# Kernel tuning notes

Hardware: AMD Instinct MI355X
Metric: run time of the kernel (lower is better)

## Reference

```python
import jax, jax.numpy as jnp
import numpy as np


def setup_inputs() -> dict:
    key = jax.random.key(0)
    B, M, S, H, D = 1, 32768, 512, 8, 64
    ks = jax.random.split(key, 5)
    f = lambda k, shape: jax.random.normal(k, shape, dtype=jnp.float32)
    return {
        "mem_keys": f(ks[0], (B, M, H, D)),
        "mem_vals": f(ks[1], (B, M, H, D)),
        "keys": f(ks[2], (B, S, H, D)),
        "values": f(ks[3], (B, S, H, D)),
        "queries": f(ks[4], (B, S, H, D)),
        "start_of_sequence": jnp.zeros((B,), dtype=jnp.bool_),
        "write_index": 0,
    }


def reference(mem_keys, mem_vals, keys, values, queries, start_of_sequence, write_index):
    """DenseKVMemory: start_segment (clear), read (joint attention), end_segment (scatter write).

    Returns (y, new_mem_keys, new_mem_vals, new_write_index).
    """
    B, S, H, D = keys.shape
    M = mem_keys.shape[1]
    dtype = mem_keys.dtype

    # --- start_segment: clear memory at document boundaries ---
    keep = jnp.logical_not(start_of_sequence).astype(dtype).reshape(B, 1, 1, 1)
    mem_keys_c = mem_keys * keep
    mem_vals_c = mem_vals * keep

    # --- read: joint attention over [memory (no mask), segment (causal mask)] ---
    scale = float(D) ** -0.5  # default 1/sqrt(head_size) when attention_scale_factor is None
    q = queries * jnp.asarray(scale, dtype)
    mem_logits = jnp.einsum('bqhd,bkhd->bhqk', q, mem_keys_c)  # [B,H,S,M]
    seg_logits = jnp.einsum('bqhd,bkhd->bhqk', q, keys)        # [B,H,S,S]

    # kq_pos = key_pos - (query_pos + queries_offset); queries_offset = 0 at segment start.
    # causal_mask True (kq_pos < 0): key strictly before query -> allowed.
    kq_pos = jnp.arange(S)[None, :] - jnp.arange(S)[:, None]
    causal_mask = kq_pos < 0  # [S,S]
    neg_inf = jnp.asarray(jnp.finfo(dtype).min, dtype)
    seg_logits = jnp.where(causal_mask[None, None, :, :], seg_logits, neg_inf)

    all_logits = jnp.concatenate([mem_logits, seg_logits], axis=-1)  # [B,H,S,M+S]
    weights = jax.nn.softmax(all_logits, axis=-1)
    all_vals = jnp.concatenate([mem_vals_c, values], axis=1)         # [B,M+S,H,D]
    y = jnp.einsum('bhqk,bkhd->bqhd', weights, all_vals)             # [B,S,H,D]

    # --- end_segment: scatter-write segment KV into the ring buffer ---
    wi = jnp.asarray(write_index, jnp.int32)
    new_mem_keys = jax.lax.dynamic_update_slice_in_dim(mem_keys_c, keys, wi, axis=1)
    new_mem_vals = jax.lax.dynamic_update_slice_in_dim(mem_vals_c, values, wi, axis=1)
    new_write_index = (wi + S) % M
    return (y, new_mem_keys, new_mem_vals, new_write_index)
```

## Files before the change

### kernel.cpp

```cpp
#include <hip/hip_runtime.h>
#include <hip/hip_bf16.h>

typedef __bf16 bf16x8 __attribute__((ext_vector_type(8)));
typedef __bf16 bf16x4 __attribute__((ext_vector_type(4)));
typedef __bf16 bf16x2 __attribute__((ext_vector_type(2)));
typedef float f32x4 __attribute__((ext_vector_type(4)));

#define M_MEM 32768
#define S_SEG 512
#define H_ 8
#define D_ 64
#define NKEY 33280
#define NTILES 520
#define LOG2E 1.44269504088896340736f
#define CMAX (14.0f * LOG2E)

#define Y_OFF 0
#define NK_OFF 262144
#define WI_OFF (262144 + 2 * 16777216)

__global__ __launch_bounds__(256, 4) void fused_attn(
    const float* __restrict__ memk, const float* __restrict__ memv,
    const float* __restrict__ keys, const float* __restrict__ vals,
    const float* __restrict__ qry, const unsigned char* __restrict__ sos,
    const int* __restrict__ wip, float* __restrict__ out,
    float* __restrict__ opart, float* __restrict__ lst, int NC) {
  const int bid = blockIdx.x;
  const int tid = threadIdx.x;
  const int c = bid >> 6;
  const int qt = (bid >> 3) & 7;
  const int h = bid & 7;
  const int w = tid >> 6;
  const int lane = tid & 63;
  const int L = lane & 15;
  const int quad = lane >> 4;
  const float keep = sos[0] ? 0.0f : 1.0f;

  int wi_raw = wip[0];
  int wi = wi_raw < 0 ? 0 : (wi_raw > M_MEM - S_SEG ? M_MEM - S_SEG : wi_raw);
  if (bid == 0 && tid == 0) {
    int nwi = (int)(((long long)wi_raw + S_SEG) % M_MEM);
    if (nwi < 0) nwi += M_MEM;
    out[WI_OFF] = (float)nwi;
  }

  __shared__ __align__(16) __bf16 Ks[64 * 72];
  __shared__ __align__(16) __bf16 Vt[64 * 72];
  __shared__ __align__(16) __bf16 Pt[4][16 * 64];

  const int qrow_base = qt * 64 + w * 16;
  const int q_abs = qrow_base + L;

  bf16x8 qf[2];
  {
    const float* qp = qry + ((size_t)q_abs * H_ + h) * D_;
    const float qs = 0.125f * LOG2E;
#pragma unroll
    for (int kb = 0; kb < 2; ++kb) {
      const int d = kb * 32 + quad * 8;
      float4 x0 = *(const float4*)(qp + d);
      float4 x1 = *(const float4*)(qp + d + 4);
      bf16x8 f;
      f[0] = (__bf16)(x0.x * qs); f[1] = (__bf16)(x0.y * qs);
      f[2] = (__bf16)(x0.z * qs); f[3] = (__bf16)(x0.w * qs);
      f[4] = (__bf16)(x1.x * qs); f[5] = (__bf16)(x1.y * qs);
      f[6] = (__bf16)(x1.z * qs); f[7] = (__bf16)(x1.w * qs);
      qf[kb] = f;
    }
  }

  f32x4 acc[4];
#pragma unroll
  for (int g = 0; g < 4; ++g) acc[g] = (f32x4){0.f, 0.f, 0.f, 0.f};
  float l_acc = 0.f;

  const int tile_start = (NTILES * c) / NC;
  const int tile_end = (NTILES * (c + 1)) / NC;
  const int nt = tile_end - tile_start;

  const int kk = tid >> 2;
  const int d0 = (tid & 3) * 16;
  const int vp2 = tid & 31;
  const int dvb = (tid >> 5) * 8;

  float4 kreg[4], vreg[4];
  float mult;
  auto issue = [&](int t) {
    const int tb = (tile_start + t) * 64;
    const float *kb_, *vb_;
    if (tb < M_MEM) {
      kb_ = memk + (size_t)tb * 512 + h * 64;
      vb_ = memv + (size_t)tb * 512 + h * 64;
      mult = keep;
    } else {
      kb_ = keys + (size_t)(tb - M_MEM) * 512 + h * 64;
      vb_ = vals + (size_t)(tb - M_MEM) * 512 + h * 64;
      mult = 1.0f;
    }
    const float* ks = kb_ + (size_t)kk * 512 + d0;
#pragma unroll
    for (int i = 0; i < 4; ++i) kreg[i] = *(const float4*)(ks + i * 4);
    const float* vs = vb_ + (size_t)(2 * vp2) * 512 + dvb;
    vreg[0] = *(const float4*)(vs);
    vreg[1] = *(const float4*)(vs + 4);
    vreg[2] = *(const float4*)(vs + 512);
    vreg[3] = *(const float4*)(vs + 516);
  };

  issue(0);
  for (int t = 0; t < nt; ++t) {
    const int tb = (tile_start + t) * 64;
    const float mu = mult;
    {
      bf16x8 lo, hi;
      lo[0] = (__bf16)(kreg[0].x * mu); lo[1] = (__bf16)(kreg[0].y * mu);
      lo[2] = (__bf16)(kreg[0].z * mu); lo[3] = (__bf16)(kreg[0].w * mu);
      lo[4] = (__bf16)(kreg[1].x * mu); lo[5] = (__bf16)(kreg[1].y * mu);
      lo[6] = (__bf16)(kreg[1].z * mu); lo[7] = (__bf16)(kreg[1].w * mu);
      hi[0] = (__bf16)(kreg[2].x * mu); hi[1] = (__bf16)(kreg[2].y * mu);
      hi[2] = (__bf16)(kreg[2].z * mu); hi[3] = (__bf16)(kreg[2].w * mu);
      hi[4] = (__bf16)(kreg[3].x * mu); hi[5] = (__bf16)(kreg[3].y * mu);
      hi[6] = (__bf16)(kreg[3].z * mu); hi[7] = (__bf16)(kreg[3].w * mu);
      *(bf16x8*)&Ks[kk * 72 + d0] = lo;
      *(bf16x8*)&Ks[kk * 72 + d0 + 8] = hi;
      const int col = (2 * vp2 + dvb) & 63;
      float a0[8] = {vreg[0].x, vreg[0].y, vreg[0].z, vreg[0].w,
                     vreg[1].x, vreg[1].y, vreg[1].z, vreg[1].w};
      float a1[8] = {vreg[2].x, vreg[2].y, vreg[2].z, vreg[2].w,
                     vreg[3].x, vreg[3].y, vreg[3].z, vreg[3].w};
#pragma unroll
      for (int i = 0; i < 8; ++i) {
        bf16x2 pr;
        pr[0] = (__bf16)(a0[i] * mu);
        pr[1] = (__bf16)(a1[i] * mu);
        *(bf16x2*)&Vt[(dvb + i) * 72 + col] = pr;
      }
      if ((((unsigned)(tb >> 6)) & 7u) == (unsigned)qt) {
        int krow = (tb < M_MEM) ? tb + kk : wi + (tb - M_MEM) + kk;
        bool kskip = (tb < M_MEM) && (krow >= wi && krow < wi + S_SEG);
        if (!kskip) {
          float* dK = out + NK_OFF + (size_t)krow * 512 + h * 64 + d0;
#pragma unroll
          for (int i = 0; i < 4; ++i) {
            float4 vv = kreg[i];
            vv.x *= mu; vv.y *= mu; vv.z *= mu; vv.w *= mu;
            *(float4*)(dK + i * 4) = vv;
          }
        }
        int r0 = (tb < M_MEM) ? tb + 2 * vp2 : wi + (tb - M_MEM) + 2 * vp2;
#pragma unroll
        for (int pk2 = 0; pk2 < 2; ++pk2) {
          int vrow = r0 + pk2;
          bool vskip = (tb < M_MEM) && (vrow >= wi && vrow < wi + S_SEG);
          if (!vskip) {
            float* dV = out + NK_OFF + 16777216 + (size_t)vrow * 512 + h * 64 + dvb;
            float4 u0 = vreg[pk2 * 2], u1 = vreg[pk2 * 2 + 1];
            u0.x *= mu; u0.y *= mu; u0.z *= mu; u0.w *= mu;
            *(float4*)(dV) = u0;
            *(float4*)(dV + 4) = u1;
          }
        }
      }
    }
    __syncthreads();
    if (t + 1 < nt) issue(t + 1);

    f32x4 sg[4];
#pragma unroll
    for (int g = 0; g < 4; ++g) {
      bf16x8 klo = *(bf16x8*)&Ks[(g * 16 + L) * 72 + quad * 8];
      bf16x8 khi = *(bf16x8*)&Ks[(g * 16 + L) * 72 + 32 + quad * 8];
      f32x4 z = (f32x4){0.f, 0.f, 0.f, 0.f};
      z = __builtin_amdgcn_mfma_f32_16x16x32_bf16(klo, qf[0], z, 0, 0, 0);
      sg[g] = __builtin_amdgcn_mfma_f32_16x16x32_bf16(khi, qf[1], z, 0, 0, 0);
    }

    const int prot = 8 * (L & 7);
#pragma unroll
    for (int g = 0; g < 4; ++g) {
      bf16x4 pk;
#pragma unroll
      for (int r = 0; r < 4; ++r) {
        const int kidx = tb + g * 16 + quad * 4 + r;
        float p = __builtin_amdgcn_exp2f(sg[g][r] - CMAX);
        const bool msk = (kidx >= M_MEM) && (kidx - M_MEM >= q_abs);
        p = msk ? 0.f : p;
        l_acc += p;
        pk[r] = (__bf16)p;
      }
      *(bf16x4*)&Pt[w][L * 64 + ((g * 16 + quad * 4 + prot) & 63)] = pk;
    }

    bf16x8 pb0 = *(bf16x8*)&Pt[w][L * 64 + ((quad * 8 + prot) & 63)];
    bf16x8 pb1 = *(bf16x8*)&Pt[w][L * 64 + ((32 + quad * 8 + prot) & 63)];
#pragma unroll
    for (int g = 0; g < 4; ++g) {
      const int vrot = g * 16 + 8 * (L >> 3);
      bf16x8 v0 = *(bf16x8*)&Vt[(g * 16 + L) * 72 + ((quad * 8 + vrot) & 63)];
      bf16x8 v1 = *(bf16x8*)&Vt[(g * 16 + L) * 72 + ((32 + quad * 8 + vrot) & 63)];
      acc[g] = __builtin_amdgcn_mfma_f32_16x16x32_bf16(v0, pb0, acc[g], 0, 0, 0);
      acc[g] = __builtin_amdgcn_mfma_f32_16x16x32_bf16(v1, pb1, acc[g], 0, 0, 0);
    }
    __syncthreads();
  }

  l_acc += __shfl_xor(l_acc, 16);
  l_acc += __shfl_xor(l_acc, 32);
  const size_t row = (size_t)h * S_SEG + q_abs;
#pragma unroll
  for (int g = 0; g < 4; ++g)
    *(f32x4*)&opart[(row * NC + c) * 64 + g * 16 + quad * 4] = acc[g];
  if (quad == 0) lst[row * NC + c] = l_acc;
}

__global__ __launch_bounds__(256) void combine(
    const float* __restrict__ opart, const float* __restrict__ lst,
    float* __restrict__ y, int NC) {
  const int idx = blockIdx.x * 256 + threadIdx.x;
  const int d = idx & 63;
  const int h = (idx >> 6) & 7;
  const int q = idx >> 9;
  const size_t row = (size_t)h * S_SEG + q;
  float num = 0.f, den = 0.f;
  for (int c = 0; c < NC; ++c) {
    num += opart[(row * NC + c) * 64 + d];
    den += lst[row * NC + c];
  }
  y[idx] = num / den;
}

extern "C" void kernel_launch(void* const* d_in, const int* in_sizes, int n_in,
                              void* d_out, int out_size, void* d_ws, size_t ws_size,
                              hipStream_t stream) {
  const float* memk = (const float*)d_in[0];
  const float* memv = (const float*)d_in[1];
  const float* keys = (const float*)d_in[2];
  const float* vals = (const float*)d_in[3];
  const float* qry  = (const float*)d_in[4];
  const unsigned char* sos = (const unsigned char*)d_in[5];
  const int* wip = (const int*)d_in[6];
  float* out = (float*)d_out;

  static const int cand[] = {20, 16, 10, 8, 5, 4, 2, 1};
  int NC = 1;
  for (int i = 0; i < 8; ++i) {
    size_t need = (size_t)cand[i] *
        ((size_t)H_ * S_SEG * D_ * 4 + (size_t)H_ * S_SEG * 4);
    if (need <= ws_size) { NC = cand[i]; break; }
  }

  float* opart = (float*)d_ws;
  float* lstp = opart + (size_t)H_ * S_SEG * NC * D_;

  fused_attn<<<NC * 64, 256, 0, stream>>>(
      memk, memv, keys, vals, qry, sos, wip, out, opart, lstp, NC);

  combine<<<1024, 256, 0, stream>>>(opart, lstp, out + Y_OFF, NC);
}
```

Baseline: 353.0 us.

## Process two query tiles per block to halve K/V tile loads

Each block now computes attention for 128 query rows (two 64-row groups) against every K/V tile it stages, so the key/value reads and bf16 conversions into shared memory are shared by twice as many queries. The grid uses half as many query blocks and allows more KV-split chunks (up to 40) to keep the GPU filled, with launch bounds relaxed to 3 to leave room for the doubled accumulators. A branch writes zeros to shared memory when memory is cleared instead of multiplying by the keep factor. Costs include higher register pressure, more partial results for the combine kernel, and an extra LDS wait between the two probability passes.

Result: faster. 326.4 us (-7.5%).

```diff
diff --git a/kernel.cpp b/kernel.cpp
--- a/kernel.cpp
+++ b/kernel.cpp
@@ -19,7 +19,7 @@
 #define NK_OFF 262144
 #define WI_OFF (262144 + 2 * 16777216)
 
-__global__ __launch_bounds__(256, 4) void fused_attn(
+__global__ __launch_bounds__(256, 3) void fused_attn(
     const float* __restrict__ memk, const float* __restrict__ memv,
     const float* __restrict__ keys, const float* __restrict__ vals,
     const float* __restrict__ qry, const unsigned char* __restrict__ sos,
@@ -27,8 +27,8 @@
     float* __restrict__ opart, float* __restrict__ lst, int NC) {
   const int bid = blockIdx.x;
   const int tid = threadIdx.x;
-  const int c = bid >> 6;
-  const int qt = (bid >> 3) & 7;
+  const int c = bid >> 5;
+  const int qp = (bid >> 3) & 3;
   const int h = bid & 7;
   const int w = tid >> 6;
   const int lane = tid & 63;
@@ -48,31 +48,41 @@
   __shared__ __align__(16) __bf16 Vt[64 * 72];
   __shared__ __align__(16) __bf16 Pt[4][16 * 64];
 
-  const int qrow_base = qt * 64 + w * 16;
-  const int q_abs = qrow_base + L;
-
-  bf16x8 qf[2];
+  const int qA = qp * 128 + w * 16 + L;
+  const int qB = qA + 64;
+
+  bf16x8 qfA[2], qfB[2];
   {
-    const float* qp = qry + ((size_t)q_abs * H_ + h) * D_;
     const float qs = 0.125f * LOG2E;
+    const float* qpA = qry + ((size_t)qA * H_ + h) * D_;
+    const float* qpB = qry + ((size_t)qB * H_ + h) * D_;
 #pragma unroll
     for (int kb = 0; kb < 2; ++kb) {
       const int d = kb * 32 + quad * 8;
-      float4 x0 = *(const float4*)(qp + d);
-      float4 x1 = *(const float4*)(qp + d + 4);
-      bf16x8 f;
-      f[0] = (__bf16)(x0.x * qs); f[1] = (__bf16)(x0.y * qs);
-      f[2] = (__bf16)(x0.z * qs); f[3] = (__bf16)(x0.w * qs);
-      f[4] = (__bf16)(x1.x * qs); f[5] = (__bf16)(x1.y * qs);
-      f[6] = (__bf16)(x1.z * qs); f[7] = (__bf16)(x1.w * qs);
-      qf[kb] = f;
-    }
-  }
-
-  f32x4 acc[4];
-#pragma unroll
-  for (int g = 0; g < 4; ++g) acc[g] = (f32x4){0.f, 0.f, 0.f, 0.f};
-  float l_acc = 0.f;
+      float4 a0 = *(const float4*)(qpA + d);
+      float4 a1 = *(const float4*)(qpA + d + 4);
+      float4 b0 = *(const float4*)(qpB + d);
+      float4 b1 = *(const float4*)(qpB + d + 4);
+      bf16x8 fa, fb;
+      fa[0] = (__bf16)(a0.x * qs); fa[1] = (__bf16)(a0.y * qs);
+      fa[2] = (__bf16)(a0.z * qs); fa[3] = (__bf16)(a0.w * qs);
+      fa[4] = (__bf16)(a1.x * qs); fa[5] = (__bf16)(a1.y * qs);
+      fa[6] = (__bf16)(a1.z * qs); fa[7] = (__bf16)(a1.w * qs);
+      fb[0] = (__bf16)(b0.x * qs); fb[1] = (__bf16)(b0.y * qs);
+      fb[2] = (__bf16)(b0.z * qs); fb[3] = (__bf16)(b0.w * qs);
+      fb[4] = (__bf16)(b1.x * qs); fb[5] = (__bf16)(b1.y * qs);
+      fb[6] = (__bf16)(b1.z * qs); fb[7] = (__bf16)(b1.w * qs);
+      qfA[kb] = fa; qfB[kb] = fb;
+    }
+  }
+
+  f32x4 accA[4], accB[4];
+#pragma unroll
+  for (int g = 0; g < 4; ++g) {
+    accA[g] = (f32x4){0.f, 0.f, 0.f, 0.f};
+    accB[g] = (f32x4){0.f, 0.f, 0.f, 0.f};
+  }
+  float lA = 0.f, lB = 0.f;
 
   const int tile_start = (NTILES * c) / NC;
   const int tile_end = (NTILES * (c + 1)) / NC;
@@ -111,16 +121,16 @@
   for (int t = 0; t < nt; ++t) {
     const int tb = (tile_start + t) * 64;
     const float mu = mult;
-    {
+    if (mu != 0.0f) {
       bf16x8 lo, hi;
-      lo[0] = (__bf16)(kreg[0].x * mu); lo[1] = (__bf16)(kreg[0].y * mu);
-      lo[2] = (__bf16)(kreg[0].z * mu); lo[3] = (__bf16)(kreg[0].w * mu);
-      lo[4] = (__bf16)(kreg[1].x * mu); lo[5] = (__bf16)(kreg[1].y * mu);
-      lo[6] = (__bf16)(kreg[1].z * mu); lo[7] = (__bf16)(kreg[1].w * mu);
-      hi[0] = (__bf16)(kreg[2].x * mu); hi[1] = (__bf16)(kreg[2].y * mu);
-      hi[2] = (__bf16)(kreg[2].z * mu); hi[3] = (__bf16)(kreg[2].w * mu);
-      hi[4] = (__bf16)(kreg[3].x * mu); hi[5] = (__bf16)(kreg[3].y * mu);
-      hi[6] = (__bf16)(kreg[3].z * mu); hi[7] = (__bf16)(kreg[3].w * mu);
+      lo[0] = (__bf16)kreg[0].x; lo[1] = (__bf16)kreg[0].y;
+      lo[2] = (__bf16)kreg[0].z; lo[3] = (__bf16)kreg[0].w;
+      lo[4] = (__bf16)kreg[1].x; lo[5] = (__bf16)kreg[1].y;
+      lo[6] = (__bf16)kreg[1].z; lo[7] = (__bf16)kreg[1].w;
+      hi[0] = (__bf16)kreg[2].x; hi[1] = (__bf16)kreg[2].y;
+      hi[2] = (__bf16)kreg[2].z; hi[3] = (__bf16)kreg[2].w;
+      hi[4] = (__bf16)kreg[3].x; hi[5] = (__bf16)kreg[3].y;
+      hi[6] = (__bf16)kreg[3].z; hi[7] = (__bf16)kreg[3].w;
       *(bf16x8*)&Ks[kk * 72 + d0] = lo;
       *(bf16x8*)&Ks[kk * 72 + d0 + 8] = hi;
       const int col = (2 * vp2 + dvb) & 63;
@@ -131,86 +141,132 @@
 #pragma unroll
       for (int i = 0; i < 8; ++i) {
         bf16x2 pr;
-        pr[0] = (__bf16)(a0[i] * mu);
-        pr[1] = (__bf16)(a1[i] * mu);
+        pr[0] = (__bf16)a0[i];
+        pr[1] = (__bf16)a1[i];
         *(bf16x2*)&Vt[(dvb + i) * 72 + col] = pr;
       }
-      if ((((unsigned)(tb >> 6)) & 7u) == (unsigned)qt) {
-        int krow = (tb < M_MEM) ? tb + kk : wi + (tb - M_MEM) + kk;
-        bool kskip = (tb < M_MEM) && (krow >= wi && krow < wi + S_SEG);
-        if (!kskip) {
-          float* dK = out + NK_OFF + (size_t)krow * 512 + h * 64 + d0;
-#pragma unroll
-          for (int i = 0; i < 4; ++i) {
-            float4 vv = kreg[i];
-            vv.x *= mu; vv.y *= mu; vv.z *= mu; vv.w *= mu;
-            *(float4*)(dK + i * 4) = vv;
-          }
+    } else {
+      bf16x8 zk = {};
+      *(bf16x8*)&Ks[kk * 72 + d0] = zk;
+      *(bf16x8*)&Ks[kk * 72 + d0 + 8] = zk;
+      const int col = (2 * vp2 + dvb) & 63;
+      bf16x2 z2 = {};
+#pragma unroll
+      for (int i = 0; i < 8; ++i) *(bf16x2*)&Vt[(dvb + i) * 72 + col] = z2;
+    }
+    if ((((unsigned)(tb >> 6)) & 3u) == (unsigned)qp) {
+      int krow = (tb < M_MEM) ? tb + kk : wi + (tb - M_MEM) + kk;
+      bool kskip = (tb < M_MEM) && (krow >= wi && krow < wi + S_SEG);
+      if (!kskip) {
+        float* dK = out + NK_OFF + (size_t)krow * 512 + h * 64 + d0;
+#pragma unroll
+        for (int i = 0; i < 4; ++i) {
+          float4 vv = kreg[i];
+          vv.x *= mu; vv.y *= mu; vv.z *= mu; vv.w *= mu;
+          *(float4*)(dK + i * 4) = vv;
         }
-        int r0 = (tb < M_MEM) ? tb + 2 * vp2 : wi + (tb - M_MEM) + 2 * vp2;
-#pragma unroll
-        for (int pk2 = 0; pk2 < 2; ++pk2) {
-          int vrow = r0 + pk2;
-          bool vskip = (tb < M_MEM) && (vrow >= wi && vrow < wi + S_SEG);
-          if (!vskip) {
-            float* dV = out + NK_OFF + 16777216 + (size_t)vrow * 512 + h * 64 + dvb;
-            float4 u0 = vreg[pk2 * 2], u1 = vreg[pk2 * 2 + 1];
-            u0.x *= mu; u0.y *= mu; u0.z *= mu; u0.w *= mu;
-            *(float4*)(dV) = u0;
-            *(float4*)(dV + 4) = u1;
-          }
+      }
+      int r0 = (tb < M_MEM) ? tb + 2 * vp2 : wi + (tb - M_MEM) + 2 * vp2;
+#pragma unroll
+      for (int pk2 = 0; pk2 < 2; ++pk2) {
+        int vrow = r0 + pk2;
+        bool vskip = (tb < M_MEM) && (vrow >= wi && vrow < wi + S_SEG);
+        if (!vskip) {
+          float* dV = out + NK_OFF + 16777216 + (size_t)vrow * 512 + h * 64 + dvb;
+          float4 u0 = vreg[pk2 * 2], u1 = vreg[pk2 * 2 + 1];
+          u0.x *= mu; u0.y *= mu; u0.z *= mu; u0.w *= mu;
+          *(float4*)(dV) = u0;
+          *(float4*)(dV + 4) = u1;
         }
       }
     }
     __syncthreads();
     if (t + 1 < nt) issue(t + 1);
 
-    f32x4 sg[4];
+    f32x4 sgA[4], sgB[4];
 #pragma unroll
     for (int g = 0; g < 4; ++g) {
       bf16x8 klo = *(bf16x8*)&Ks[(g * 16 + L) * 72 + quad * 8];
       bf16x8 khi = *(bf16x8*)&Ks[(g * 16 + L) * 72 + 32 + quad * 8];
-      f32x4 z = (f32x4){0.f, 0.f, 0.f, 0.f};
-      z = __builtin_amdgcn_mfma_f32_16x16x32_bf16(klo, qf[0], z, 0, 0, 0);
-      sg[g] = __builtin_amdgcn_mfma_f32_16x16x32_bf16(khi, qf[1], z, 0, 0, 0);
+      f32x4 zA = (f32x4){0.f, 0.f, 0.f, 0.f};
+      f32x4 zB = (f32x4){0.f, 0.f, 0.f, 0.f};
+      zA = __builtin_amdgcn_mfma_f32_16x16x32_bf16(klo, qfA[0], zA, 0, 0, 0);
+      zB = __builtin_amdgcn_mfma_f32_16x16x32_bf16(klo, qfB[0], zB, 0, 0, 0);
+      sgA[g] = __builtin_amdgcn_mfma_f32_16x16x32_bf16(khi, qfA[1], zA, 0, 0, 0);
+      sgB[g] = __builtin_amdgcn_mfma_f32_16x16x32_bf16(khi, qfB[1], zB, 0, 0, 0);
     }
 
     const int prot = 8 * (L & 7);
+    const bool segt = (tb >= M_MEM);
 #pragma unroll
     for (int g = 0; g < 4; ++g) {
       bf16x4 pk;
 #pragma unroll
       for (int r = 0; r < 4; ++r) {
-        const int kidx = tb + g * 16 + quad * 4 + r;
-        float p = __builtin_amdgcn_exp2f(sg[g][r] - CMAX);
-        const bool msk = (kidx >= M_MEM) && (kidx - M_MEM >= q_abs);
-        p = msk ? 0.f : p;
-        l_acc += p;
+        float p = __builtin_amdgcn_exp2f(sgA[g][r] - CMAX);
+        if (segt) {
+          const int kseg = tb - M_MEM + g * 16 + quad * 4 + r;
+          p = (kseg >= qA) ? 0.f : p;
+        }
+        lA += p;
         pk[r] = (__bf16)p;
       }
       *(bf16x4*)&Pt[w][L * 64 + ((g * 16 + quad * 4 + prot) & 63)] = pk;
     }
-
-    bf16x8 pb0 = *(bf16x8*)&Pt[w][L * 64 + ((quad * 8 + prot) & 63)];
-    bf16x8 pb1 = *(bf16x8*)&Pt[w][L * 64 + ((32 + quad * 8 + prot) & 63)];
+    bf16x8 pbA0 = *(bf16x8*)&Pt[w][L * 64 + ((quad * 8 + prot) & 63)];
+    bf16x8 pbA1 = *(bf16x8*)&Pt[w][L * 64 + ((32 + quad * 8 + prot) & 63)];
+
+    bf16x4 pkB[4];
+#pragma unroll
+    for (int g = 0; g < 4; ++g) {
+      bf16x4 pk;
+#pragma unroll
+      for (int r = 0; r < 4; ++r) {
+        float p = __builtin_amdgcn_exp2f(sgB[g][r] - CMAX);
+        if (segt) {
+          const int kseg = tb - M_MEM + g * 16 + quad * 4 + r;
+          p = (kseg >= qB) ? 0.f : p;
+        }
+        lB += p;
+        pk[r] = (__bf16)p;
+      }
+      pkB[g] = pk;
+    }
+    asm volatile("s_waitcnt lgkmcnt(0)" ::: "memory");
+#pragma unroll
+    for (int g = 0; g < 4; ++g)
+      *(bf16x4*)&Pt[w][L * 64 + ((g * 16 + quad * 4 + prot) & 63)] = pkB[g];
+    bf16x8 pbB0 = *(bf16x8*)&Pt[w][L * 64 + ((quad * 8 + prot) & 63)];
+    bf16x8 pbB1 = *(bf16x8*)&Pt[w][L * 64 + ((32 + quad * 8 + prot) & 63)];
+
 #pragma unroll
     for (int g = 0; g < 4; ++g) {
       const int vrot = g * 16 + 8 * (L >> 3);
       bf16x8 v0 = *(bf16x8*)&Vt[(g * 16 + L) * 72 + ((quad * 8 + vrot) & 63)];
       bf16x8 v1 = *(bf16x8*)&Vt[(g * 16 + L) * 72 + ((32 + quad * 8 + vrot) & 63)];
-      acc[g] = __builtin_amdgcn_mfma_f32_16x16x32_bf16(v0, pb0, acc[g], 0, 0, 0);
-      acc[g] = __builtin_amdgcn_mfma_f32_16x16x32_bf16(v1, pb1, acc[g], 0, 0, 0);
+      accA[g] = __builtin_amdgcn_mfma_f32_16x16x32_bf16(v0, pbA0, accA[g], 0, 0, 0);
+      accA[g] = __builtin_amdgcn_mfma_f32_16x16x32_bf16(v1, pbA1, accA[g], 0, 0, 0);
+      accB[g] = __builtin_amdgcn_mfma_f32_16x16x32_bf16(v0, pbB0, accB[g], 0, 0, 0);
+      accB[g] = __builtin_amdgcn_mfma_f32_16x16x32_bf16(v1, pbB1, accB[g], 0, 0, 0);
     }
     __syncthreads();
   }
 
-  l_acc += __shfl_xor(l_acc, 16);
-  l_acc += __shfl_xor(l_acc, 32);
-  const size_t row = (size_t)h * S_SEG + q_abs;
-#pragma unroll
-  for (int g = 0; g < 4; ++g)
-    *(f32x4*)&opart[(row * NC + c) * 64 + g * 16 + quad * 4] = acc[g];
-  if (quad == 0) lst[row * NC + c] = l_acc;
+  lA += __shfl_xor(lA, 16);
+  lA += __shfl_xor(lA, 32);
+  lB += __shfl_xor(lB, 16);
+  lB += __shfl_xor(lB, 32);
+  const size_t rowA = (size_t)h * S_SEG + qA;
+  const size_t rowB = (size_t)h * S_SEG + qB;
+#pragma unroll
+  for (int g = 0; g < 4; ++g) {
+    *(f32x4*)&opart[(rowA * NC + c) * 64 + g * 16 + quad * 4] = accA[g];
+    *(f32x4*)&opart[(rowB * NC + c) * 64 + g * 16 + quad * 4] = accB[g];
+  }
+  if (quad == 0) {
+    lst[rowA * NC + c] = lA;
+    lst[rowB * NC + c] = lB;
+  }
 }
 
 __global__ __launch_bounds__(256) void combine(
@@ -241,9 +297,9 @@
   const int* wip = (const int*)d_in[6];
   float* out = (float*)d_out;
 
-  static const int cand[] = {20, 16, 10, 8, 5, 4, 2, 1};
+  static const int cand[] = {40, 32, 24, 20, 16, 10, 8, 5, 4, 2, 1};
   int NC = 1;
-  for (int i = 0; i < 8; ++i) {
+  for (int i = 0; i < 11; ++i) {
     size_t need = (size_t)cand[i] *
         ((size_t)H_ * S_SEG * D_ * 4 + (size_t)H_ * S_SEG * 4);
     if (need <= ws_size) { NC = cand[i]; break; }
@@ -252,7 +308,7 @@
   float* opart = (float*)d_ws;
   float* lstp = opart + (size_t)H_ * S_SEG * NC * D_;
 
-  fused_attn<<<NC * 64, 256, 0, stream>>>(
+  fused_attn<<<NC * 32, 256, 0, stream>>>(
       memk, memv, keys, vals, qry, sos, wip, out, opart, lstp, NC);
 
   combine<<<1024, 256, 0, stream>>>(opart, lstp, out + Y_OFF, NC);
```
